# Kernel optimization log

Measured on AMD Instinct MI355X. Metric: run time of the kernel, lower is better.

The kernel has to match this reference:

```python
import jax, jax.numpy as jnp
import numpy as np

TURBO_BLOCK_SIZE = 64
TURBO_MSE_BITS = 5
QMAX = 2 ** (TURBO_MSE_BITS - 1) - 1  # 15 for symmetric int5
# MSE scale search grid: shrink factors applied to the max-abs scale
SHRINKS = np.linspace(0.4, 1.0, 16)


def mse_quant_dequant(w):
    """Block-wise (block=64, along input dim) symmetric int5 quantize-dequantize.
    Per block, searches a grid of shrunken max-abs scales and keeps the one
    minimizing reconstruction MSE."""
    O, I = w.shape
    wb = w.reshape(O, I // TURBO_BLOCK_SIZE, TURBO_BLOCK_SIZE)
    amax = jnp.max(jnp.abs(wb), axis=-1, keepdims=True)
    base = jnp.maximum(amax, 1e-8) / QMAX
    best_err = jnp.full(amax.shape, jnp.inf, dtype=w.dtype)
    best_scale = base
    for s in SHRINKS:  # fixed small grid, not a data-dim loop
        scale = base * jnp.asarray(s, dtype=w.dtype)
        deq = jnp.clip(jnp.round(wb / scale), -QMAX, QMAX) * scale
        err = jnp.sum((deq - wb) ** 2, axis=-1, keepdims=True)
        upd = err < best_err
        best_err = jnp.where(upd, err, best_err)
        best_scale = jnp.where(upd, scale, best_scale)
    deq = jnp.clip(jnp.round(wb / best_scale), -QMAX, QMAX) * best_scale
    return deq.reshape(O, I)


def turbo_linear(x, w):
    # Straight-through estimator: forward uses quantized weights,
    # gradient flows to w as identity.
    wq = w + jax.lax.stop_gradient(mse_quant_dequant(w) - w)
    return x @ wq.T


def setup_inputs() -> dict:
    key = jax.random.key(0)
    k1, k2, k3 = jax.random.split(key, 3)
    dim, mlp_mult = 2048, 4
    hidden = mlp_mult * dim
    x = jax.random.normal(k1, (4, 2048, dim), dtype=jnp.float32)
    w_fc = jax.random.normal(k2, (hidden, dim), dtype=jnp.float32) * 0.02
    w_proj = jax.random.normal(k3, (dim, hidden), dtype=jnp.float32) * 0.02
    return {"x": x, "w_fc": w_fc, "w_proj": w_proj}


def reference(x, w_fc, w_proj):
    h = jnp.maximum(turbo_linear(x, w_fc), 0.0)  # relu
    return turbo_linear(h * h, w_proj)           # relu-square then proj
```

## Files before the change

kernel.cpp:

```cpp
#include <hip/hip_runtime.h>
#include <hip/hip_bf16.h>

typedef __attribute__((ext_vector_type(8))) __bf16 bf16x8;
typedef __attribute__((ext_vector_type(4))) float f32x4;

__device__ __forceinline__ void gload_lds16(const void* g, void* lds) {
    __builtin_amdgcn_global_load_lds(
        (const __attribute__((address_space(1))) void*)g,
        (__attribute__((address_space(3))) void*)lds, 16, 0, 0);
}

__global__ __launch_bounds__(256) void quant_bf16_kernel(
    const float* __restrict__ w, __hip_bfloat16* __restrict__ wq, int nblk)
{
#pragma clang fp contract(off)
    int b = blockIdx.x * 256 + threadIdx.x;
    if (b >= nblk) return;
    const float4* src = (const float4*)(w + (size_t)b * 64);
    float v[64];
#pragma unroll
    for (int i = 0; i < 16; ++i) {
        float4 t = src[i];
        v[i*4+0] = t.x; v[i*4+1] = t.y; v[i*4+2] = t.z; v[i*4+3] = t.w;
    }
    float amax = 0.0f;
#pragma unroll
    for (int i = 0; i < 64; ++i) amax = fmaxf(amax, fabsf(v[i]));
    float base = fmaxf(amax, 1e-8f) / 15.0f;

    float best_err = __builtin_inff();
    float best_scale = base, best_rs = 0.0f;
    for (int k = 0; k < 16; ++k) {
        double sd = (k == 15) ? 1.0 : ((double)k * (0.6 / 15.0) + 0.4);
        float scale = base * (float)sd;
        float rs = 1.0f / scale;
        float err = 0.0f;
#pragma unroll
        for (int i = 0; i < 64; ++i) {
            float q = rintf(v[i] * rs);
            q = fminf(fmaxf(q, -15.0f), 15.0f);
            float d = q * scale - v[i];
            err = err + d * d;
        }
        if (err < best_err) { best_err = err; best_scale = scale; best_rs = rs; }
    }
    __hip_bfloat16* dst = wq + (size_t)b * 64;
#pragma unroll
    for (int i = 0; i < 64; ++i) {
        float q = rintf(v[i] * best_rs);
        q = fminf(fmaxf(q, -15.0f), 15.0f);
        dst[i] = __float2bfloat16(q * best_scale);
    }
}

__global__ __launch_bounds__(256) void f32_to_bf16_kernel(
    const float* __restrict__ in, __hip_bfloat16* __restrict__ out, int n8)
{
    int i = blockIdx.x * 256 + threadIdx.x;
    if (i >= n8) return;
    const float4* p = (const float4*)(in + (size_t)i * 8);
    float4 a = p[0], b = p[1];
    alignas(16) __hip_bfloat16 r[8];
    r[0] = __float2bfloat16(a.x); r[1] = __float2bfloat16(a.y);
    r[2] = __float2bfloat16(a.z); r[3] = __float2bfloat16(a.w);
    r[4] = __float2bfloat16(b.x); r[5] = __float2bfloat16(b.y);
    r[6] = __float2bfloat16(b.z); r[7] = __float2bfloat16(b.w);
    *(uint4*)(out + (size_t)i * 8) = *(const uint4*)r;
}

template <int EPI>
__global__ __launch_bounds__(512, 1) void gemm256_kernel(
    const __hip_bfloat16* __restrict__ A,
    const __hip_bfloat16* __restrict__ B,
    void* __restrict__ Cout, int M, int N, int K)
{
    extern __shared__ char smem[];

    const int t    = threadIdx.x;
    const int lane = t & 63;
    const int w    = t >> 6;
    const int wr   = w >> 2;
    const int wc   = w & 3;
    const int lo   = lane & 15;
    const int hi   = lane >> 4;
    const uint wOff = (uint)w * 1024u;

    const int cpx = gridDim.x >> 3;
    int bid = blockIdx.x;
    bid = (bid & 7) * cpx + (bid >> 3);
    const int nN = N >> 8;
    const int bm = bid / nN;
    const int bn = bid % nN;
    const int rowBase = bm << 8;
    const int colBase = bn << 8;

    uint offA0, offA1, offB0, offB1;
    {
        uint o0 = (uint)t * 16u;
        uint o1 = 8192u + (uint)t * 16u;
        uint p0 = o0 ^ (((o0 >> 7) & 7u) << 4);
        uint p1 = o1 ^ (((o1 >> 7) & 7u) << 4);
        uint r0 = p0 >> 7, c0 = (p0 & 127u) >> 1;
        uint r1 = p1 >> 7, c1 = (p1 & 127u) >> 1;
        offA0 = (uint)(rowBase + r0) * (uint)K + c0;
        offA1 = (uint)(rowBase + r1) * (uint)K + c1;
        offB0 = (uint)(colBase + r0) * (uint)K + c0;
        offB1 = (uint)(colBase + r1) * (uint)K + c1;
    }
    const uint hG = 128u * (uint)K;

    const uint sw  = (uint)(lo & 7) << 4;
    const uint aB  = (uint)wr * 16384u + (uint)lo * 128u;
    const uint bB  = 32768u + (uint)(wc >> 1) * 16384u
                   + ((uint)(wc & 1) * 64u + (uint)lo) * 128u;
    const uint cb0 = ((uint)hi * 16u) ^ sw;
    const uint cb1 = (64u + (uint)hi * 16u) ^ sw;

    f32x4 acc[8][4] = {};
    bf16x8 bfrag[4][2];

    gload_lds16(A + (size_t)offA0,        smem + 0     + wOff);
    gload_lds16(A + (size_t)offA1,        smem + 8192  + wOff);
    gload_lds16(A + (size_t)(offA0 + hG), smem + 16384 + wOff);
    gload_lds16(A + (size_t)(offA1 + hG), smem + 24576 + wOff);
    gload_lds16(B + (size_t)offB0,        smem + 32768 + wOff);
    gload_lds16(B + (size_t)offB1,        smem + 40960 + wOff);
    gload_lds16(B + (size_t)(offB0 + hG), smem + 49152 + wOff);
    gload_lds16(B + (size_t)(offB1 + hG), smem + 57344 + wOff);
    gload_lds16(B + (size_t)(offB0 + 64),      smem + 65536 + 32768 + wOff);
    gload_lds16(B + (size_t)(offB1 + 64),      smem + 65536 + 40960 + wOff);
    gload_lds16(B + (size_t)(offB0 + hG + 64), smem + 65536 + 49152 + wOff);
    gload_lds16(B + (size_t)(offB1 + hG + 64), smem + 65536 + 57344 + wOff);
    asm volatile("s_waitcnt vmcnt(4)" ::: "memory");
    __builtin_amdgcn_s_barrier();

    const int NI = K >> 7;
    for (int P = 0; P < NI; ++P) {
        const bool pf = (P + 1 < NI);
        const uint kN1 = ((uint)(2 * P + 1)) << 6;
        const uint kN2 = kN1 + 64;
        const uint kN3 = kN1 + 128;
#pragma unroll
        for (int ph = 0; ph < 8; ++ph) {
            const int q = ph & 3;
            const uint bufOff = (uint)(ph >> 2) * 65536u;
            bf16x8 afrag[2][2];
#pragma unroll
            for (int di = 0; di < 2; ++di) {
                const uint ab = bufOff + aB + (uint)(2 * q + di) * 2048u;
                afrag[di][0] = *(const bf16x8*)(smem + ab + cb0);
                afrag[di][1] = *(const bf16x8*)(smem + ab + cb1);
            }
            if (q == 0) {
#pragma unroll
                for (int j = 0; j < 4; ++j) {
                    const uint bb = bufOff + bB + (uint)j * 2048u;
                    bfrag[j][0] = *(const bf16x8*)(smem + bb + cb0);
                    bfrag[j][1] = *(const bf16x8*)(smem + bb + cb1);
                }
            }
            if (ph == 0) {
                gload_lds16(A + (size_t)(offA0 + kN1), smem + 65536 + 0    + wOff);
                gload_lds16(A + (size_t)(offA1 + kN1), smem + 65536 + 8192 + wOff);
            } else if (ph == 1) {
                gload_lds16(A + (size_t)(offA0 + hG + kN1), smem + 65536 + 16384 + wOff);
                gload_lds16(A + (size_t)(offA1 + hG + kN1), smem + 65536 + 24576 + wOff);
            } else if (ph == 2) { if (pf) {
                gload_lds16(B + (size_t)(offB0 + kN2), smem + 32768 + wOff);
                gload_lds16(B + (size_t)(offB1 + kN2), smem + 40960 + wOff); }
            } else if (ph == 3) { if (pf) {
                gload_lds16(B + (size_t)(offB0 + hG + kN2), smem + 49152 + wOff);
                gload_lds16(B + (size_t)(offB1 + hG + kN2), smem + 57344 + wOff); }
            } else if (ph == 4) { if (pf) {
                gload_lds16(A + (size_t)(offA0 + kN2), smem + 0    + wOff);
                gload_lds16(A + (size_t)(offA1 + kN2), smem + 8192 + wOff); }
            } else if (ph == 5) { if (pf) {
                gload_lds16(A + (size_t)(offA0 + hG + kN2), smem + 16384 + wOff);
                gload_lds16(A + (size_t)(offA1 + hG + kN2), smem + 24576 + wOff); }
            } else if (ph == 6) { if (pf) {
                gload_lds16(B + (size_t)(offB0 + kN3), smem + 65536 + 32768 + wOff);
                gload_lds16(B + (size_t)(offB1 + kN3), smem + 65536 + 40960 + wOff); }
            } else { if (pf) {
                gload_lds16(B + (size_t)(offB0 + hG + kN3), smem + 65536 + 49152 + wOff);
                gload_lds16(B + (size_t)(offB1 + hG + kN3), smem + 65536 + 57344 + wOff); }
            }

            __builtin_amdgcn_s_barrier();
            asm volatile("s_waitcnt lgkmcnt(0)" ::: "memory");
            __builtin_amdgcn_s_setprio(1);
#pragma unroll
            for (int di = 0; di < 2; ++di)
#pragma unroll
                for (int j = 0; j < 4; ++j) {
                    acc[2*q+di][j] = __builtin_amdgcn_mfma_f32_16x16x32_bf16(
                        afrag[di][0], bfrag[j][0], acc[2*q+di][j], 0, 0, 0);
                    acc[2*q+di][j] = __builtin_amdgcn_mfma_f32_16x16x32_bf16(
                        afrag[di][1], bfrag[j][1], acc[2*q+di][j], 0, 0, 0);
                }
            __builtin_amdgcn_s_setprio(0);
            if (ph == 3) {
                if (pf) asm volatile("s_waitcnt vmcnt(4)" ::: "memory");
                else    asm volatile("s_waitcnt vmcnt(0)" ::: "memory");
            } else if (ph == 7) {
                if (pf) asm volatile("s_waitcnt vmcnt(4)" ::: "memory");
            }
            __builtin_amdgcn_s_barrier();
        }
    }

    if (EPI == 0) {
        __hip_bfloat16* Cb = (__hip_bfloat16*)Cout;
#pragma unroll
        for (int i = 0; i < 8; ++i)
#pragma unroll
            for (int j = 0; j < 4; ++j)
#pragma unroll
                for (int r = 0; r < 4; ++r) {
                    size_t row = rowBase + wr*128 + i*16 + hi*4 + r;
                    size_t col = colBase + wc*64 + j*16 + lo;
                    float v = fmaxf(acc[i][j][r], 0.0f);
                    Cb[row * N + col] = __float2bfloat16(v * v);
                }
    } else {
        float* Cf = (float*)Cout;
#pragma unroll
        for (int i = 0; i < 8; ++i)
#pragma unroll
            for (int j = 0; j < 4; ++j)
#pragma unroll
                for (int r = 0; r < 4; ++r) {
                    size_t row = rowBase + wr*128 + i*16 + hi*4 + r;
                    size_t col = colBase + wc*64 + j*16 + lo;
                    Cf[row * N + col] = acc[i][j][r];
                }
    }
}

extern "C" void kernel_launch(void* const* d_in, const int* in_sizes, int n_in,
                              void* d_out, int out_size, void* d_ws, size_t ws_size,
                              hipStream_t stream) {
    const float* x      = (const float*)d_in[0];
    const float* w_fc   = (const float*)d_in[1];
    const float* w_proj = (const float*)d_in[2];
    float* out = (float*)d_out;

    const int DIM = 2048, HID = 8192, M = 8192;

    char* ws = (char*)d_ws;
    __hip_bfloat16* Xb  = (__hip_bfloat16*)ws;
    __hip_bfloat16* Wfc = (__hip_bfloat16*)(ws + (size_t)M * DIM * 2);
    __hip_bfloat16* Wpj = (__hip_bfloat16*)(ws + (size_t)(M * DIM + (size_t)HID * DIM) * 2);
    __hip_bfloat16* H2  = (__hip_bfloat16*)(ws + (size_t)(M * DIM + 2 * (size_t)HID * DIM) * 2);

    (void)hipFuncSetAttribute((const void*)gemm256_kernel<0>,
                              hipFuncAttributeMaxDynamicSharedMemorySize, 131072);
    (void)hipFuncSetAttribute((const void*)gemm256_kernel<1>,
                              hipFuncAttributeMaxDynamicSharedMemorySize, 131072);

    int nblk = HID * DIM / 64;
    quant_bf16_kernel<<<nblk / 256, 256, 0, stream>>>(w_fc, Wfc, nblk);
    quant_bf16_kernel<<<nblk / 256, 256, 0, stream>>>(w_proj, Wpj, nblk);

    int n8 = M * DIM / 8;
    f32_to_bf16_kernel<<<n8 / 256, 256, 0, stream>>>(x, Xb, n8);

    gemm256_kernel<0><<<(M/256)*(HID/256), 512, 131072, stream>>>(
        Xb, Wfc, (void*)H2, M, HID, DIM);

    gemm256_kernel<1><<<(M/256)*(DIM/256), 512, 131072, stream>>>(
        H2, Wpj, (void*)out, M, DIM, HID);
}
```

Before: 611.3 us.

## Software-pipeline LDS fragment loads behind MFMAs with one barrier per phase

Restructures the GEMM main loop into explicit phases where the A/B LDS fragments for the next phase are loaded while the current MFMAs run, replacing the per-phase lgkmcnt(0) wait and double barrier with a single barrier. Global-to-LDS address math is simplified to a single per-thread offset plus K*64 strides. vmcnt thresholds are adjusted to the new staging order. This aims to hide LDS latency and cut barrier overhead, at the cost of extra fragment registers and tighter correctness dependence on hand-placed waits.

```diff
diff --git a/kernel.cpp b/kernel.cpp
--- a/kernel.cpp
+++ b/kernel.cpp
@@ -68,6 +68,36 @@
     *(uint4*)(out + (size_t)i * 8) = *(const uint4*)r;
 }
 
+#define LDA2(d, base, s) { \
+    d[0] = *(const bf16x8*)(smem + (base) + aB + (s)*2048u + cb0); \
+    d[1] = *(const bf16x8*)(smem + (base) + aB + (s)*2048u + cb1); }
+
+#define LDB8(base) { \
+    bf[0][0] = *(const bf16x8*)(smem + (base) + bB + 0u    + cb0); \
+    bf[0][1] = *(const bf16x8*)(smem + (base) + bB + 0u    + cb1); \
+    bf[1][0] = *(const bf16x8*)(smem + (base) + bB + 2048u + cb0); \
+    bf[1][1] = *(const bf16x8*)(smem + (base) + bB + 2048u + cb1); \
+    bf[2][0] = *(const bf16x8*)(smem + (base) + bB + 4096u + cb0); \
+    bf[2][1] = *(const bf16x8*)(smem + (base) + bB + 4096u + cb1); \
+    bf[3][0] = *(const bf16x8*)(smem + (base) + bB + 6144u + cb0); \
+    bf[3][1] = *(const bf16x8*)(smem + (base) + bB + 6144u + cb1); }
+
+#define MF8(q, a2) { \
+    acc[q][0] = __builtin_amdgcn_mfma_f32_16x16x32_bf16(a2[0], bf[0][0], acc[q][0],0,0,0); \
+    acc[q][0] = __builtin_amdgcn_mfma_f32_16x16x32_bf16(a2[1], bf[0][1], acc[q][0],0,0,0); \
+    acc[q][1] = __builtin_amdgcn_mfma_f32_16x16x32_bf16(a2[0], bf[1][0], acc[q][1],0,0,0); \
+    acc[q][1] = __builtin_amdgcn_mfma_f32_16x16x32_bf16(a2[1], bf[1][1], acc[q][1],0,0,0); \
+    acc[q][2] = __builtin_amdgcn_mfma_f32_16x16x32_bf16(a2[0], bf[2][0], acc[q][2],0,0,0); \
+    acc[q][2] = __builtin_amdgcn_mfma_f32_16x16x32_bf16(a2[1], bf[2][1], acc[q][2],0,0,0); \
+    acc[q][3] = __builtin_amdgcn_mfma_f32_16x16x32_bf16(a2[0], bf[3][0], acc[q][3],0,0,0); \
+    acc[q][3] = __builtin_amdgcn_mfma_f32_16x16x32_bf16(a2[1], bf[3][1], acc[q][3],0,0,0); }
+
+#define STAGE(base, eoff, ldsOff) \
+    gload_lds16((base) + (size_t)((eoff) + voff), smem + (ldsOff) + wOff)
+
+#define BARRIER() { __builtin_amdgcn_sched_barrier(0); \
+    __builtin_amdgcn_s_barrier(); __builtin_amdgcn_sched_barrier(0); }
+
 template <int EPI>
 __global__ __launch_bounds__(512, 1) void gemm256_kernel(
     const __hip_bfloat16* __restrict__ A,
@@ -94,20 +124,12 @@
     const int rowBase = bm << 8;
     const int colBase = bn << 8;
 
-    uint offA0, offA1, offB0, offB1;
-    {
-        uint o0 = (uint)t * 16u;
-        uint o1 = 8192u + (uint)t * 16u;
-        uint p0 = o0 ^ (((o0 >> 7) & 7u) << 4);
-        uint p1 = o1 ^ (((o1 >> 7) & 7u) << 4);
-        uint r0 = p0 >> 7, c0 = (p0 & 127u) >> 1;
-        uint r1 = p1 >> 7, c1 = (p1 & 127u) >> 1;
-        offA0 = (uint)(rowBase + r0) * (uint)K + c0;
-        offA1 = (uint)(rowBase + r1) * (uint)K + c1;
-        offB0 = (uint)(colBase + r0) * (uint)K + c0;
-        offB1 = (uint)(colBase + r1) * (uint)K + c1;
-    }
-    const uint hG = 128u * (uint)K;
+    const __hip_bfloat16* uA = A + (size_t)rowBase * (size_t)K;
+    const __hip_bfloat16* uB = B + (size_t)colBase * (size_t)K;
+    uint o0 = (uint)t * 16u;
+    uint p0 = o0 ^ (((o0 >> 7) & 7u) << 4);
+    const uint voff = (p0 >> 7) * (uint)K + ((p0 & 127u) >> 1);
+    const uint K64 = (uint)K * 64u;
 
     const uint sw  = (uint)(lo & 7) << 4;
     const uint aB  = (uint)wr * 16384u + (uint)lo * 128u;
@@ -117,95 +139,85 @@
     const uint cb1 = (64u + (uint)hi * 16u) ^ sw;
 
     f32x4 acc[8][4] = {};
-    bf16x8 bfrag[4][2];
-
-    gload_lds16(A + (size_t)offA0,        smem + 0     + wOff);
-    gload_lds16(A + (size_t)offA1,        smem + 8192  + wOff);
-    gload_lds16(A + (size_t)(offA0 + hG), smem + 16384 + wOff);
-    gload_lds16(A + (size_t)(offA1 + hG), smem + 24576 + wOff);
-    gload_lds16(B + (size_t)offB0,        smem + 32768 + wOff);
-    gload_lds16(B + (size_t)offB1,        smem + 40960 + wOff);
-    gload_lds16(B + (size_t)(offB0 + hG), smem + 49152 + wOff);
-    gload_lds16(B + (size_t)(offB1 + hG), smem + 57344 + wOff);
-    gload_lds16(B + (size_t)(offB0 + 64),      smem + 65536 + 32768 + wOff);
-    gload_lds16(B + (size_t)(offB1 + 64),      smem + 65536 + 40960 + wOff);
-    gload_lds16(B + (size_t)(offB0 + hG + 64), smem + 65536 + 49152 + wOff);
-    gload_lds16(B + (size_t)(offB1 + hG + 64), smem + 65536 + 57344 + wOff);
+    bf16x8 aC0[2], aC1[2], bf[4][2];
+
+    STAGE(uA, 0u,        0u);       STAGE(uA, K64,        8192u);
+    STAGE(uA, 2u*K64,    16384u);   STAGE(uA, 3u*K64,     24576u);
+    STAGE(uB, 0u,        32768u);   STAGE(uB, K64,        40960u);
+    STAGE(uB, 2u*K64,    49152u);   STAGE(uB, 3u*K64,     57344u);
+    STAGE(uB, 64u,           98304u);  STAGE(uB, K64 + 64u,     106496u);
+    STAGE(uB, 2u*K64 + 64u, 114688u);  STAGE(uB, 3u*K64 + 64u,  122880u);
     asm volatile("s_waitcnt vmcnt(4)" ::: "memory");
-    __builtin_amdgcn_s_barrier();
+    BARRIER();
+    LDA2(aC0, 0u, 0u); LDA2(aC1, 0u, 1u); LDB8(0u);
 
     const int NI = K >> 7;
     for (int P = 0; P < NI; ++P) {
         const bool pf = (P + 1 < NI);
         const uint kN1 = ((uint)(2 * P + 1)) << 6;
-        const uint kN2 = kN1 + 64;
-        const uint kN3 = kN1 + 128;
-#pragma unroll
-        for (int ph = 0; ph < 8; ++ph) {
-            const int q = ph & 3;
-            const uint bufOff = (uint)(ph >> 2) * 65536u;
-            bf16x8 afrag[2][2];
-#pragma unroll
-            for (int di = 0; di < 2; ++di) {
-                const uint ab = bufOff + aB + (uint)(2 * q + di) * 2048u;
-                afrag[di][0] = *(const bf16x8*)(smem + ab + cb0);
-                afrag[di][1] = *(const bf16x8*)(smem + ab + cb1);
-            }
-            if (q == 0) {
-#pragma unroll
-                for (int j = 0; j < 4; ++j) {
-                    const uint bb = bufOff + bB + (uint)j * 2048u;
-                    bfrag[j][0] = *(const bf16x8*)(smem + bb + cb0);
-                    bfrag[j][1] = *(const bf16x8*)(smem + bb + cb1);
-                }
-            }
-            if (ph == 0) {
-                gload_lds16(A + (size_t)(offA0 + kN1), smem + 65536 + 0    + wOff);
-                gload_lds16(A + (size_t)(offA1 + kN1), smem + 65536 + 8192 + wOff);
-            } else if (ph == 1) {
-                gload_lds16(A + (size_t)(offA0 + hG + kN1), smem + 65536 + 16384 + wOff);
-                gload_lds16(A + (size_t)(offA1 + hG + kN1), smem + 65536 + 24576 + wOff);
-            } else if (ph == 2) { if (pf) {
-                gload_lds16(B + (size_t)(offB0 + kN2), smem + 32768 + wOff);
-                gload_lds16(B + (size_t)(offB1 + kN2), smem + 40960 + wOff); }
-            } else if (ph == 3) { if (pf) {
-                gload_lds16(B + (size_t)(offB0 + hG + kN2), smem + 49152 + wOff);
-                gload_lds16(B + (size_t)(offB1 + hG + kN2), smem + 57344 + wOff); }
-            } else if (ph == 4) { if (pf) {
-                gload_lds16(A + (size_t)(offA0 + kN2), smem + 0    + wOff);
-                gload_lds16(A + (size_t)(offA1 + kN2), smem + 8192 + wOff); }
-            } else if (ph == 5) { if (pf) {
-                gload_lds16(A + (size_t)(offA0 + hG + kN2), smem + 16384 + wOff);
-                gload_lds16(A + (size_t)(offA1 + hG + kN2), smem + 24576 + wOff); }
-            } else if (ph == 6) { if (pf) {
-                gload_lds16(B + (size_t)(offB0 + kN3), smem + 65536 + 32768 + wOff);
-                gload_lds16(B + (size_t)(offB1 + kN3), smem + 65536 + 40960 + wOff); }
-            } else { if (pf) {
-                gload_lds16(B + (size_t)(offB0 + hG + kN3), smem + 65536 + 49152 + wOff);
-                gload_lds16(B + (size_t)(offB1 + hG + kN3), smem + 65536 + 57344 + wOff); }
-            }
-
-            __builtin_amdgcn_s_barrier();
-            asm volatile("s_waitcnt lgkmcnt(0)" ::: "memory");
-            __builtin_amdgcn_s_setprio(1);
-#pragma unroll
-            for (int di = 0; di < 2; ++di)
-#pragma unroll
-                for (int j = 0; j < 4; ++j) {
-                    acc[2*q+di][j] = __builtin_amdgcn_mfma_f32_16x16x32_bf16(
-                        afrag[di][0], bfrag[j][0], acc[2*q+di][j], 0, 0, 0);
-                    acc[2*q+di][j] = __builtin_amdgcn_mfma_f32_16x16x32_bf16(
-                        afrag[di][1], bfrag[j][1], acc[2*q+di][j], 0, 0, 0);
-                }
-            __builtin_amdgcn_s_setprio(0);
-            if (ph == 3) {
-                if (pf) asm volatile("s_waitcnt vmcnt(4)" ::: "memory");
-                else    asm volatile("s_waitcnt vmcnt(0)" ::: "memory");
-            } else if (ph == 7) {
-                if (pf) asm volatile("s_waitcnt vmcnt(4)" ::: "memory");
-            }
-            __builtin_amdgcn_s_barrier();
-        }
+        const uint kN2 = kN1 + 64u;
+        const uint kN3 = kN1 + 128u;
+
+        STAGE(uA, kN1,       65536u);  STAGE(uA, kN1 + K64, 73728u);
+        __builtin_amdgcn_s_setprio(1);
+        MF8(0, aC0); LDA2(aC0, 0u, 2u);
+        MF8(1, aC1); LDA2(aC1, 0u, 3u);
+        __builtin_amdgcn_s_setprio(0);
+        BARRIER();
+
+        STAGE(uA, kN1 + 2u*K64, 81920u);  STAGE(uA, kN1 + 3u*K64, 90112u);
+        __builtin_amdgcn_s_setprio(1);
+        MF8(2, aC0); LDA2(aC0, 0u, 4u);
+        MF8(3, aC1); LDA2(aC1, 0u, 5u);
+        __builtin_amdgcn_s_setprio(0);
+        BARRIER();
+
+        if (pf) { STAGE(uB, kN2, 32768u); STAGE(uB, kN2 + K64, 40960u); }
+        __builtin_amdgcn_s_setprio(1);
+        MF8(4, aC0); LDA2(aC0, 0u, 6u);
+        MF8(5, aC1); LDA2(aC1, 0u, 7u);
+        __builtin_amdgcn_s_setprio(0);
+        if (pf) asm volatile("s_waitcnt vmcnt(2)" ::: "memory");
+        else    asm volatile("s_waitcnt vmcnt(0)" ::: "memory");
+        BARRIER();
+
+        if (pf) { STAGE(uB, kN2 + 2u*K64, 49152u); STAGE(uB, kN2 + 3u*K64, 57344u); }
+        __builtin_amdgcn_s_setprio(1);
+        MF8(6, aC0); LDA2(aC0, 65536u, 0u);
+        MF8(7, aC1); LDA2(aC1, 65536u, 1u);
+        __builtin_amdgcn_s_setprio(0);
+        LDB8(65536u);
+        BARRIER();
+
+        if (pf) { STAGE(uA, kN2, 0u); STAGE(uA, kN2 + K64, 8192u); }
+        __builtin_amdgcn_s_setprio(1);
+        MF8(0, aC0); LDA2(aC0, 65536u, 2u);
+        MF8(1, aC1); LDA2(aC1, 65536u, 3u);
+        __builtin_amdgcn_s_setprio(0);
+        BARRIER();
+
+        if (pf) { STAGE(uA, kN2 + 2u*K64, 16384u); STAGE(uA, kN2 + 3u*K64, 24576u); }
+        __builtin_amdgcn_s_setprio(1);
+        MF8(2, aC0); LDA2(aC0, 65536u, 4u);
+        MF8(3, aC1); LDA2(aC1, 65536u, 5u);
+        __builtin_amdgcn_s_setprio(0);
+        BARRIER();
+
+        if (pf) { STAGE(uB, kN3, 98304u); STAGE(uB, kN3 + K64, 106496u); }
+        __builtin_amdgcn_s_setprio(1);
+        MF8(4, aC0); LDA2(aC0, 65536u, 6u);
+        MF8(5, aC1); LDA2(aC1, 65536u, 7u);
+        __builtin_amdgcn_s_setprio(0);
+        if (pf) asm volatile("s_waitcnt vmcnt(2)" ::: "memory");
+        BARRIER();
+
+        if (pf) { STAGE(uB, kN3 + 2u*K64, 114688u); STAGE(uB, kN3 + 3u*K64, 122880u); }
+        __builtin_amdgcn_s_setprio(1);
+        MF8(6, aC0); if (pf) LDA2(aC0, 0u, 0u);
+        MF8(7, aC1); if (pf) LDA2(aC1, 0u, 1u);
+        __builtin_amdgcn_s_setprio(0);
+        if (pf) LDB8(0u);
+        BARRIER();
     }
 
     if (EPI == 0) {
```

Measured after the change: 590.1 us. 1.04x faster.
